# Performance work log

Measured on AMD Instinct MI355X. Metric: run time of the kernel, lower is better.

The kernel has to match this reference:

```python
import jax, jax.numpy as jnp
import numpy as np

N, K, G, C, H = 4096, 32, 1, 96, 6
HD = C // H
POS_BND = int(0.8 * K)      # 25 (dilation=1)
RPE_NUM = 2 * POS_BND + 1   # 51
SCALE = HD ** -0.5


def setup_inputs() -> dict:
    key = jax.random.key(0)
    ks = jax.random.split(key, 6)
    return {
        "data": jax.random.normal(ks[0], (N, K + G, C), jnp.float32),
        "rel_pos": jax.random.randint(ks[1], (N, K, K, 3), 0, RPE_NUM, jnp.int32),
        "mask": jnp.zeros((N, K + G, K + G), jnp.float32),
        "qkv_w": jax.random.normal(ks[2], (C, 3 * C), jnp.float32) * 0.05,
        "qkv_b": jnp.zeros((3 * C,), jnp.float32),
        "proj_w": jax.random.normal(ks[3], (C, C), jnp.float32) * 0.05,
        "proj_b": jnp.zeros((C,), jnp.float32),
        "rpe_table": jax.random.normal(ks[4], (3 * RPE_NUM, H), jnp.float32) * 0.02,
    }


def _rpe_lookup(rel_pos, rpe_table):
    # rel_pos holds uniform indices in [0, RPE_NUM); center to [-POS_BND, POS_BND]
    xyz = rel_pos - POS_BND
    xyz = jnp.clip(xyz, -POS_BND, POS_BND)
    idx = xyz + POS_BND + jnp.arange(3, dtype=rel_pos.dtype) * RPE_NUM  # [N,K,K,3]
    rpe = rpe_table[idx].sum(axis=3)   # gather table -> [N,K,K,3,H] -> sum xyz -> [N,K,K,H]
    return rpe.transpose(0, 3, 1, 2)   # [N,H,K,K]


def reference(data, rel_pos, mask, qkv_w, qkv_b, proj_w, proj_b, rpe_table):
    # data: [N, K+G, C] windowed tokens with G relay tokens already prepended
    qkv = (data @ qkv_w + qkv_b).reshape(N, K + G, 3, H, HD)
    qkv = qkv.transpose(2, 0, 3, 1, 4)               # [3, N, H, K+G, HD]
    q, k, v = qkv[0] * SCALE, qkv[1], qkv[2]
    attn = jnp.einsum('nhqd,nhkd->nhqk', q, k)       # [N, H, K+G, K+G]
    rpe = _rpe_lookup(rel_pos, rpe_table)            # [N, H, K, K]
    rpe = jnp.pad(rpe, ((0, 0), (0, 0), (G, 0), (G, 0)))  # F.pad(rpe,(G,0,G,0))
    attn = attn + rpe + mask[:, None]                # additive HAT window mask
    attn = jax.nn.softmax(attn, axis=-1)
    out = jnp.einsum('nhqk,nhkd->nhqd', attn, v)
    out = out.transpose(0, 2, 1, 3).reshape(N, K + G, C)
    return out @ proj_w + proj_b
```

## Files before the change

### kernel.cpp

```cpp
#include <hip/hip_runtime.h>
#include <cstdint>


static constexpr int NWIN = 4096;
static constexpr int MROWS = NWIN * 33;
static constexpr float SCALE = 0.25f;
static constexpr int KVSTRIDE = 7008;

using short8 = __attribute__((ext_vector_type(8))) short;
using f32x4  = __attribute__((ext_vector_type(4))) float;

__device__ __forceinline__ unsigned short f2bf(float f) {
  unsigned u = __float_as_uint(f);
  u += 0x7fffu + ((u >> 16) & 1u);
  return (unsigned short)(u >> 16);
}
__device__ __forceinline__ float bf2f(unsigned short h) {
  return __uint_as_float(((unsigned)h) << 16);
}
__device__ __forceinline__ float bflo(unsigned u) { return __uint_as_float(u << 16); }
__device__ __forceinline__ float bfhi(unsigned u) { return __uint_as_float(u & 0xffff0000u); }

__global__ __launch_bounds__(256) void conv_w_qkv(
    const float* __restrict__ W, unsigned* __restrict__ frag) {
  const int fp = blockIdx.x;
  const int kstep = fp / 36;
  const int r = fp - kstep*36;
  const int cf = r >> 1, hl = r & 1;
  const int t = threadIdx.x, lane = t >> 2, d = t & 3;
  const int k = kstep*32 + (lane >> 4)*8 + d*2;
  const int n = cf*16 + (lane & 15);
  float w0 = W[k*288 + n], w1 = W[(k+1)*288 + n];
  if (hl) { w0 -= bf2f(f2bf(w0)); w1 -= bf2f(f2bf(w1)); }
  frag[fp*256 + t] = (unsigned)f2bf(w0) | ((unsigned)f2bf(w1) << 16);
}

__global__ __launch_bounds__(256) void conv_w_proj(
    const float* __restrict__ W, unsigned* __restrict__ frag) {
  const int fp = blockIdx.x;
  const int kstep = fp / 12;
  const int r = fp - kstep*12;
  const int cf = r >> 1, hl = r & 1;
  const int t = threadIdx.x, lane = t >> 2, d = t & 3;
  const int k = kstep*32 + (lane >> 4)*8 + d*2;
  const int n = cf*16 + (lane & 15);
  float w0 = W[k*96 + n], w1 = W[(k+1)*96 + n];
  if (hl) { w0 -= bf2f(f2bf(w0)); w1 -= bf2f(f2bf(w1)); }
  frag[fp*256 + t] = (unsigned)f2bf(w0) | ((unsigned)f2bf(w1) << 16);
}

__global__ __launch_bounds__(256) void qkv_mfma(
    const float* __restrict__ A, const unsigned* __restrict__ frag,
    const float* __restrict__ bias, float* __restrict__ qf,
    unsigned short* __restrict__ kvh) {
  __shared__ __align__(16) unsigned short sBuf[13056];
  unsigned short* sAh = sBuf;
  unsigned short* sAl = sBuf + 5120;
  const int tid = threadIdx.x;
  const int w = tid >> 6, l = tid & 63;
  const int m0 = blockIdx.x * 128;
  const int s = blockIdx.y;
  f32x4 acc[2][6];
  #pragma unroll
  for (int rf = 0; rf < 2; ++rf)
    #pragma unroll
    for (int cf = 0; cf < 6; ++cf) acc[rf][cf] = (f32x4){0.f,0.f,0.f,0.f};

  #pragma unroll
  for (int kstep = 0; kstep < 3; ++kstep) {
    short8 bh[6], bl[6];
    #pragma unroll
    for (int cf = 0; cf < 6; ++cf) {
      const int fp = (kstep*18 + s*6 + cf)*2;
      bh[cf] = *(const short8*)((const char*)frag + (size_t)fp*1024 + l*16);
      bl[cf] = *(const short8*)((const char*)frag + (size_t)fp*1024 + 1024 + l*16);
    }
    __syncthreads();
    #pragma unroll
    for (int it2 = 0; it2 < 4; ++it2) {
      const int idx = tid + it2*256;
      const int row = idx >> 3, q = idx & 7;
      const float4 v = *(const float4*)(A + (size_t)(m0+row)*96 + kstep*32 + q*4);
      ushort4 hv, lv;
      hv.x = f2bf(v.x); hv.y = f2bf(v.y); hv.z = f2bf(v.z); hv.w = f2bf(v.w);
      lv.x = f2bf(v.x - bf2f(hv.x)); lv.y = f2bf(v.y - bf2f(hv.y));
      lv.z = f2bf(v.z - bf2f(hv.z)); lv.w = f2bf(v.w - bf2f(hv.w));
      *(ushort4*)&sAh[row*40 + q*4] = hv;
      *(ushort4*)&sAl[row*40 + q*4] = lv;
    }
    __syncthreads();
    #pragma unroll
    for (int rf = 0; rf < 2; ++rf) {
      const int row = w*32 + rf*16 + (l & 15);
      const int off = row*40 + (l >> 4)*8;
      const short8 ah = *(const short8*)&sAh[off];
      const short8 al = *(const short8*)&sAl[off];
      #pragma unroll
      for (int cf = 0; cf < 6; ++cf) {
        acc[rf][cf] = __builtin_amdgcn_mfma_f32_16x16x32_bf16(ah, bh[cf], acc[rf][cf], 0,0,0);
        acc[rf][cf] = __builtin_amdgcn_mfma_f32_16x16x32_bf16(al, bh[cf], acc[rf][cf], 0,0,0);
        acc[rf][cf] = __builtin_amdgcn_mfma_f32_16x16x32_bf16(ah, bl[cf], acc[rf][cf], 0,0,0);
      }
    }
  }
  const int col = l & 15;
  if (s == 0) {
    #pragma unroll
    for (int cf = 0; cf < 6; ++cf) {
      const float bv = bias[cf*16 + col];
      #pragma unroll
      for (int rf = 0; rf < 2; ++rf)
        #pragma unroll
        for (int r = 0; r < 4; ++r) {
          const int m = m0 + w*32 + rf*16 + (l >> 4)*4 + r;
          const int n = m / 33, t = m - n*33;
          qf[(size_t)n*3168 + cf*528 + t*16 + col] = (acc[rf][cf][r] + bv)*SCALE;
        }
    }
  } else if (s == 1) {
    #pragma unroll
    for (int cf = 0; cf < 6; ++cf) {
      const float bv = bias[96 + cf*16 + col];
      #pragma unroll
      for (int rf = 0; rf < 2; ++rf)
        #pragma unroll
        for (int r = 0; r < 4; ++r) {
          const int m = m0 + w*32 + rf*16 + (l >> 4)*4 + r;
          const int n = m / 33, t = m - n*33;
          kvh[(size_t)n*KVSTRIDE + cf*528 + t*16 + col] = f2bf(acc[rf][cf][r] + bv);
        }
    }
  } else {
    __syncthreads();
    unsigned short* sV = sBuf;
    #pragma unroll
    for (int cf = 0; cf < 6; ++cf) {
      const float bv = bias[192 + cf*16 + col];
      #pragma unroll
      for (int rf = 0; rf < 2; ++rf)
        #pragma unroll
        for (int r = 0; r < 4; ++r) {
          const int row = w*32 + rf*16 + (l >> 4)*4 + r;
          sV[row*102 + cf*16 + col] = f2bf(acc[rf][cf][r] + bv);
        }
    }
    __syncthreads();
    for (int idx = tid; idx < 12288; idx += 256) {
      const int hd = idx >> 7, trow = idx & 127;
      const int m = m0 + trow;
      const int n = m / 33, t = m - n*33;
      kvh[(size_t)n*KVSTRIDE + 3168 + (hd >> 4)*640 + (hd & 15)*40 + t] =
          sV[trow*102 + hd];
    }
  }
}

__global__ __launch_bounds__(384) void attn_kernel(
    float* __restrict__ qf, const unsigned short* __restrict__ kvh,
    const int* __restrict__ rel, const float* __restrict__ mask,
    const float* __restrict__ rpet) {
  __shared__ __align__(8) unsigned short sBiasH[7168];
  __shared__ __align__(4) unsigned short sRpe6[920];
  const int tid = threadIdx.x;
  const int n = blockIdx.x;
  const int l = tid & 63, g = l >> 4, c = l & 15, h = tid >> 6;
  const unsigned short* Kb = kvh + (size_t)n*KVSTRIDE + h*528;
  const unsigned short* Vb = kvh + (size_t)n*KVSTRIDE + 3168 + h*640;
  const float*          Qb = qf  + (size_t)n*3168 + h*528;
  short8 ka[3];
  #pragma unroll
  for (int jt = 0; jt < 3; ++jt)
    ka[jt] = *(const short8*)(Kb + (jt*16 + c)*16 + (g & 1)*8);
  const short8 vb8 = *(const short8*)(Vb + c*40 + g*8);
  const unsigned short v32u = Vb[c*40 + 32];
  float4 qa_[3], qc_[3];
  #pragma unroll
  for (int it = 0; it < 3; ++it) {
    const int i = it*16 + c;
    qa_[it] = make_float4(0.f,0.f,0.f,0.f);
    qc_[it] = make_float4(0.f,0.f,0.f,0.f);
    if (i < 33) {
      qa_[it] = *(const float4*)(Qb + i*16 + (g & 1)*8);
      qc_[it] = *(const float4*)(Qb + i*16 + (g & 1)*8 + 4);
    }
  }
  for (int idx = tid; idx < 918; idx += 384) sRpe6[idx] = f2bf(rpet[idx]);
  __syncthreads();
  {
    const float* gm = mask + (size_t)n*1089;
    const int*   rb = rel  + (size_t)n*3072;
    const unsigned* rp6 = (const unsigned*)sRpe6;
    int   ee[3];
    bool  act[3], rpok[3];
    float mv[3];
    int   xx[3][3];
    #pragma unroll
    for (int q2 = 0; q2 < 3; ++q2) {
      int e = tid + q2*384;
      act[q2] = (e < 1089);
      if (!act[q2]) e = 0;
      ee[q2] = e;
      const int i = e / 33, j = e - i*33;
      rpok[q2] = (i > 0) && (j > 0);
      const int rbase = rpok[q2] ? ((i-1)*32 + (j-1))*3 : 0;
      mv[q2]    = gm[e];
      xx[q2][0] = rb[rbase]*3;
      xx[q2][1] = (rb[rbase+1] + 51)*3;
      xx[q2][2] = (rb[rbase+2] + 102)*3;
    }
    #pragma unroll
    for (int q2 = 0; q2 < 3; ++q2) {
      float b0=0.f, b1=0.f, b2=0.f, b3=0.f, b4=0.f, b5=0.f;
      #pragma unroll
      for (int a = 0; a < 3; ++a) {
        const unsigned u0 = rp6[xx[q2][a]];
        const unsigned u1 = rp6[xx[q2][a]+1];
        const unsigned u2 = rp6[xx[q2][a]+2];
        b0 += bflo(u0); b1 += bfhi(u0);
        b2 += bflo(u1); b3 += bfhi(u1);
        b4 += bflo(u2); b5 += bfhi(u2);
      }
      const float m2 = mv[q2];
      const bool ok = rpok[q2];
      b0 = ok ? b0 + m2 : m2;  b1 = ok ? b1 + m2 : m2;
      b2 = ok ? b2 + m2 : m2;  b3 = ok ? b3 + m2 : m2;
      b4 = ok ? b4 + m2 : m2;  b5 = ok ? b5 + m2 : m2;
      if (act[q2]) {
        const int e = ee[q2];
        const int i = e / 33, j = e - i*33;
        const int bb = i*36 + j;
        sBiasH[bb]        = f2bf(b0);
        sBiasH[bb + 1188] = f2bf(b1);
        sBiasH[bb + 2376] = f2bf(b2);
        sBiasH[bb + 3564] = f2bf(b3);
        sBiasH[bb + 4752] = f2bf(b4);
        sBiasH[bb + 5940] = f2bf(b5);
      }
    }
  }
  const float v32f = bf2f(v32u);
  short8 qfr[3];
  #pragma unroll
  for (int it = 0; it < 3; ++it) {
    const float qv[8] = {qa_[it].x, qa_[it].y, qa_[it].z, qa_[it].w,
                         qc_[it].x, qc_[it].y, qc_[it].z, qc_[it].w};
    short8 t;
    #pragma unroll
    for (int e = 0; e < 8; ++e) {
      const unsigned short hi = f2bf(qv[e]);
      const unsigned short lo = f2bf(qv[e] - bf2f(hi));
      t[e] = (short)((g < 2) ? hi : lo);
    }
    qfr[it] = t;
  }
  __syncthreads();
  const int hbase = h*1188;
  #pragma unroll
  for (int it = 0; it < 3; ++it) {
    const int i  = it*16 + c;
    const int bi = (i < 33) ? i : 0;
    const int bbase = hbase + bi*36;
    float pv[12];
    float mx = -3.4e38f;
    #pragma unroll
    for (int jt = 0; jt < 3; ++jt) {
      const ushort4 bv4 = *(const ushort4*)(sBiasH + bbase + jt*16 + 4*g);
      f32x4 sacc;
      sacc[0] = bf2f(bv4.x); sacc[1] = bf2f(bv4.y);
      sacc[2] = bf2f(bv4.z); sacc[3] = bf2f(bv4.w);
      sacc = __builtin_amdgcn_mfma_f32_16x16x32_bf16(ka[jt], qfr[it], sacc, 0,0,0);
      #pragma unroll
      for (int r = 0; r < 4; ++r) {
        const int j = jt*16 + 4*g + r;
        float sv = sacc[r];
        if (j >= 33) sv = -3.4e38f;
        pv[jt*4+r] = sv;
        mx = fmaxf(mx, sv);
      }
    }
    mx = fmaxf(mx, __shfl_xor(mx, 16));
    mx = fmaxf(mx, __shfl_xor(mx, 32));
    float ss = 0.f;
    #pragma unroll
    for (int e = 0; e < 12; ++e) { pv[e] = __expf(pv[e] - mx); ss += pv[e]; }
    ss += __shfl_xor(ss, 16);
    ss += __shfl_xor(ss, 32);
    const float inv = 1.0f / ss;
    const unsigned t0d0 = (unsigned)f2bf(pv[0]*inv) | ((unsigned)f2bf(pv[1]*inv) << 16);
    const unsigned t0d1 = (unsigned)f2bf(pv[2]*inv) | ((unsigned)f2bf(pv[3]*inv) << 16);
    const unsigned t1d0 = (unsigned)f2bf(pv[4]*inv) | ((unsigned)f2bf(pv[5]*inv) << 16);
    const unsigned t1d1 = (unsigned)f2bf(pv[6]*inv) | ((unsigned)f2bf(pv[7]*inv) << 16);
    const int L0 = (((g << 1) & 3) << 4) | c;
    const int L1 = ((((g << 1) | 1) & 3) << 4) | c;
    const unsigned s00 = (unsigned)__shfl((int)t0d0, L0);
    const unsigned s01 = (unsigned)__shfl((int)t0d1, L0);
    const unsigned s02 = (unsigned)__shfl((int)t1d0, L0);
    const unsigned s03 = (unsigned)__shfl((int)t1d1, L0);
    const unsigned s10 = (unsigned)__shfl((int)t0d0, L1);
    const unsigned s11 = (unsigned)__shfl((int)t0d1, L1);
    const unsigned s12 = (unsigned)__shfl((int)t1d0, L1);
    const unsigned s13 = (unsigned)__shfl((int)t1d1, L1);
    const bool lo2 = (g < 2);
    uint4 av;
    av.x = lo2 ? s00 : s02;
    av.y = lo2 ? s01 : s03;
    av.z = lo2 ? s10 : s12;
    av.w = lo2 ? s11 : s13;
    const short8 pa = __builtin_bit_cast(short8, av);
    f32x4 o = (f32x4){0.f,0.f,0.f,0.f};
    o = __builtin_amdgcn_mfma_f32_16x16x32_bf16(pa, vb8, o, 0,0,0);
    const float p32f = pv[8] * inv;
    #pragma unroll
    for (int r = 0; r < 4; ++r) {
      const float p32 = __shfl(p32f, 4*g + r);
      o[r] += p32 * v32f;
    }
    float* ob = qf + (size_t)n*3168 + h*16 + c;
    #pragma unroll
    for (int r = 0; r < 4; ++r) {
      const int io = it*16 + 4*g + r;
      if (io < 33) ob[(size_t)io*96] = o[r];
    }
  }
}

__global__ __launch_bounds__(256) void proj_mfma(
    const float* __restrict__ qf, const unsigned* __restrict__ frag,
    const float* __restrict__ bias, float* __restrict__ out) {
  __shared__ __align__(16) unsigned short sAh[128*104];
  __shared__ __align__(16) unsigned short sAl[128*104];
  const int tid = threadIdx.x;
  const int w = tid >> 6, l = tid & 63;
  const int m0 = blockIdx.x * 128;
  for (int idx = tid; idx < 3072; idx += 256) {
    const int row = idx / 24, q = idx - row*24;
    const int m = m0 + row;
    const int n = m / 33, t = m - n*33;
    const float4 v = *(const float4*)(qf + (size_t)n*3168 + t*96 + q*4);
    ushort4 hv, lv;
    hv.x = f2bf(v.x); hv.y = f2bf(v.y); hv.z = f2bf(v.z); hv.w = f2bf(v.w);
    lv.x = f2bf(v.x - bf2f(hv.x)); lv.y = f2bf(v.y - bf2f(hv.y));
    lv.z = f2bf(v.z - bf2f(hv.z)); lv.w = f2bf(v.w - bf2f(hv.w));
    *(ushort4*)&sAh[row*104 + q*4] = hv;
    *(ushort4*)&sAl[row*104 + q*4] = lv;
  }
  __syncthreads();
  f32x4 acc[2][6];
  #pragma unroll
  for (int rf = 0; rf < 2; ++rf)
    #pragma unroll
    for (int cf = 0; cf < 6; ++cf) acc[rf][cf] = (f32x4){0.f,0.f,0.f,0.f};

  #pragma unroll
  for (int kstep = 0; kstep < 3; ++kstep) {
    short8 bh[6], bl[6];
    #pragma unroll
    for (int cf = 0; cf < 6; ++cf) {
      const int fph = kstep*12 + cf*2;
      bh[cf] = *(const short8*)(frag + fph*256 + l*4);
      bl[cf] = *(const short8*)(frag + (fph+1)*256 + l*4);
    }
    #pragma unroll
    for (int rf = 0; rf < 2; ++rf) {
      const int row = w*32 + rf*16 + (l & 15);
      const int off = row*104 + kstep*32 + (l >> 4)*8;
      const short8 ah = *(const short8*)&sAh[off];
      const short8 al = *(const short8*)&sAl[off];
      #pragma unroll
      for (int cf = 0; cf < 6; ++cf) {
        acc[rf][cf] = __builtin_amdgcn_mfma_f32_16x16x32_bf16(ah, bh[cf], acc[rf][cf], 0,0,0);
        acc[rf][cf] = __builtin_amdgcn_mfma_f32_16x16x32_bf16(al, bh[cf], acc[rf][cf], 0,0,0);
        acc[rf][cf] = __builtin_amdgcn_mfma_f32_16x16x32_bf16(ah, bl[cf], acc[rf][cf], 0,0,0);
      }
    }
  }
  const int col = l & 15;
  #pragma unroll
  for (int cf = 0; cf < 6; ++cf) {
    const float bv = bias[cf*16 + col];
    #pragma unroll
    for (int rf = 0; rf < 2; ++rf)
      #pragma unroll
      for (int r = 0; r < 4; ++r) {
        const int m = m0 + w*32 + rf*16 + (l >> 4)*4 + r;
        out[(size_t)m*96 + cf*16 + col] = acc[rf][cf][r] + bv;
      }
  }
}

extern "C" void kernel_launch(void* const* d_in, const int* in_sizes, int n_in,
                              void* d_out, int out_size, void* d_ws, size_t ws_size,
                              hipStream_t stream) {
  const float* data   = (const float*)d_in[0];
  const int*   rel    = (const int*)  d_in[1];
  const float* mask   = (const float*)d_in[2];
  const float* qkv_w  = (const float*)d_in[3];
  const float* qkv_b  = (const float*)d_in[4];
  const float* proj_w = (const float*)d_in[5];
  const float* proj_b = (const float*)d_in[6];
  const float* rpet   = (const float*)d_in[7];
  float* qf = (float*)d_ws;
  unsigned short* kvh = (unsigned short*)(qf + (size_t)NWIN*3168);
  float* out = (float*)d_out;

  conv_w_qkv <<<dim3(108),          256, 0, stream>>>(qkv_w, (unsigned*)d_out);
  qkv_mfma   <<<dim3(MROWS/128, 3), 256, 0, stream>>>(data, (const unsigned*)d_out, qkv_b, qf, kvh);
  attn_kernel<<<dim3(NWIN),         384, 0, stream>>>(qf, kvh, rel, mask, rpet);
  conv_w_proj<<<dim3(36),           256, 0, stream>>>(proj_w, (unsigned*)kvh);
  proj_mfma  <<<dim3(MROWS/128),    256, 0, stream>>>(qf, (const unsigned*)kvh, proj_b, out);
}
```

Measured before the change: 137.9 us.

## Split QKV GEMM into Q and fused K/V kernels; stream proj A tiles per k-step

The single 3-way blockIdx.y QKV kernel becomes two kernels. A Q kernel handles the Q projection on 128-row tiles. A KV kernel handles K and V together on 64-row tiles, reusing one A-tile conversion for both, so the input is read and split to bf16 twice instead of three times. The proj kernel now loads and splits its A tile one 32-column k-step at a time into a smaller shared buffer instead of staging all 96 columns up front, which cuts LDS use and may raise occupancy. The trade-offs are an extra kernel launch, an extra sync per k-step, and the K/V kernel doing per-wave work on 16 rows, which may lower MFMA utilisation per block.

```diff
diff --git a/kernel.cpp b/kernel.cpp
--- a/kernel.cpp
+++ b/kernel.cpp
@@ -49,17 +49,15 @@
   frag[fp*256 + t] = (unsigned)f2bf(w0) | ((unsigned)f2bf(w1) << 16);
 }
 
-__global__ __launch_bounds__(256) void qkv_mfma(
+__global__ __launch_bounds__(256) void q_mfma(
     const float* __restrict__ A, const unsigned* __restrict__ frag,
-    const float* __restrict__ bias, float* __restrict__ qf,
-    unsigned short* __restrict__ kvh) {
-  __shared__ __align__(16) unsigned short sBuf[13056];
+    const float* __restrict__ bias, float* __restrict__ qf) {
+  __shared__ __align__(16) unsigned short sBuf[10240];
   unsigned short* sAh = sBuf;
   unsigned short* sAl = sBuf + 5120;
   const int tid = threadIdx.x;
   const int w = tid >> 6, l = tid & 63;
   const int m0 = blockIdx.x * 128;
-  const int s = blockIdx.y;
   f32x4 acc[2][6];
   #pragma unroll
   for (int rf = 0; rf < 2; ++rf)
@@ -71,7 +69,7 @@
     short8 bh[6], bl[6];
     #pragma unroll
     for (int cf = 0; cf < 6; ++cf) {
-      const int fp = (kstep*18 + s*6 + cf)*2;
+      const int fp = (kstep*18 + cf)*2;
       bh[cf] = *(const short8*)((const char*)frag + (size_t)fp*1024 + l*16);
       bl[cf] = *(const short8*)((const char*)frag + (size_t)fp*1024 + 1024 + l*16);
     }
@@ -104,54 +102,110 @@
     }
   }
   const int col = l & 15;
-  if (s == 0) {
-    #pragma unroll
-    for (int cf = 0; cf < 6; ++cf) {
-      const float bv = bias[cf*16 + col];
-      #pragma unroll
-      for (int rf = 0; rf < 2; ++rf)
-        #pragma unroll
-        for (int r = 0; r < 4; ++r) {
-          const int m = m0 + w*32 + rf*16 + (l >> 4)*4 + r;
-          const int n = m / 33, t = m - n*33;
-          qf[(size_t)n*3168 + cf*528 + t*16 + col] = (acc[rf][cf][r] + bv)*SCALE;
-        }
-    }
-  } else if (s == 1) {
-    #pragma unroll
-    for (int cf = 0; cf < 6; ++cf) {
-      const float bv = bias[96 + cf*16 + col];
-      #pragma unroll
-      for (int rf = 0; rf < 2; ++rf)
-        #pragma unroll
-        for (int r = 0; r < 4; ++r) {
-          const int m = m0 + w*32 + rf*16 + (l >> 4)*4 + r;
-          const int n = m / 33, t = m - n*33;
-          kvh[(size_t)n*KVSTRIDE + cf*528 + t*16 + col] = f2bf(acc[rf][cf][r] + bv);
-        }
-    }
-  } else {
-    __syncthreads();
-    unsigned short* sV = sBuf;
-    #pragma unroll
-    for (int cf = 0; cf < 6; ++cf) {
-      const float bv = bias[192 + cf*16 + col];
-      #pragma unroll
-      for (int rf = 0; rf < 2; ++rf)
-        #pragma unroll
-        for (int r = 0; r < 4; ++r) {
-          const int row = w*32 + rf*16 + (l >> 4)*4 + r;
-          sV[row*102 + cf*16 + col] = f2bf(acc[rf][cf][r] + bv);
-        }
-    }
-    __syncthreads();
-    for (int idx = tid; idx < 12288; idx += 256) {
-      const int hd = idx >> 7, trow = idx & 127;
-      const int m = m0 + trow;
+  #pragma unroll
+  for (int cf = 0; cf < 6; ++cf) {
+    const float bv = bias[cf*16 + col];
+    #pragma unroll
+    for (int rf = 0; rf < 2; ++rf)
+      #pragma unroll
+      for (int r = 0; r < 4; ++r) {
+        const int m = m0 + w*32 + rf*16 + (l >> 4)*4 + r;
+        const int n = m / 33, t = m - n*33;
+        qf[(size_t)n*3168 + cf*528 + t*16 + col] = (acc[rf][cf][r] + bv)*SCALE;
+      }
+  }
+}
+
+__global__ __launch_bounds__(256) void kv_mfma(
+    const float* __restrict__ A, const unsigned* __restrict__ frag,
+    const float* __restrict__ bias, unsigned short* __restrict__ kvh) {
+  __shared__ __align__(16) unsigned short sBuf[6528];
+  unsigned short* sAh = sBuf;
+  unsigned short* sAl = sBuf + 2560;
+  const int tid = threadIdx.x;
+  const int w = tid >> 6, l = tid & 63;
+  const int m0 = blockIdx.x * 64;
+  f32x4 acck[6], accv[6];
+  #pragma unroll
+  for (int cf = 0; cf < 6; ++cf) {
+    acck[cf] = (f32x4){0.f,0.f,0.f,0.f};
+    accv[cf] = (f32x4){0.f,0.f,0.f,0.f};
+  }
+  #pragma unroll
+  for (int kstep = 0; kstep < 3; ++kstep) {
+    short8 bh[6], bl[6];
+    #pragma unroll
+    for (int cf = 0; cf < 6; ++cf) {
+      const int fp = (kstep*18 + 6 + cf)*2;
+      bh[cf] = *(const short8*)((const char*)frag + (size_t)fp*1024 + l*16);
+      bl[cf] = *(const short8*)((const char*)frag + (size_t)fp*1024 + 1024 + l*16);
+    }
+    __syncthreads();
+    #pragma unroll
+    for (int it2 = 0; it2 < 2; ++it2) {
+      const int idx = tid + it2*256;
+      const int row = idx >> 3, q = idx & 7;
+      const float4 v = *(const float4*)(A + (size_t)(m0+row)*96 + kstep*32 + q*4);
+      ushort4 hv, lv;
+      hv.x = f2bf(v.x); hv.y = f2bf(v.y); hv.z = f2bf(v.z); hv.w = f2bf(v.w);
+      lv.x = f2bf(v.x - bf2f(hv.x)); lv.y = f2bf(v.y - bf2f(hv.y));
+      lv.z = f2bf(v.z - bf2f(hv.z)); lv.w = f2bf(v.w - bf2f(hv.w));
+      *(ushort4*)&sAh[row*40 + q*4] = hv;
+      *(ushort4*)&sAl[row*40 + q*4] = lv;
+    }
+    __syncthreads();
+    const int row = w*16 + (l & 15);
+    const int off = row*40 + (l >> 4)*8;
+    const short8 ah = *(const short8*)&sAh[off];
+    const short8 al = *(const short8*)&sAl[off];
+    #pragma unroll
+    for (int cf = 0; cf < 6; ++cf) {
+      acck[cf] = __builtin_amdgcn_mfma_f32_16x16x32_bf16(ah, bh[cf], acck[cf], 0,0,0);
+      acck[cf] = __builtin_amdgcn_mfma_f32_16x16x32_bf16(al, bh[cf], acck[cf], 0,0,0);
+      acck[cf] = __builtin_amdgcn_mfma_f32_16x16x32_bf16(ah, bl[cf], acck[cf], 0,0,0);
+    }
+    #pragma unroll
+    for (int cf = 0; cf < 6; ++cf) {
+      const int fp = (kstep*18 + 12 + cf)*2;
+      bh[cf] = *(const short8*)((const char*)frag + (size_t)fp*1024 + l*16);
+      bl[cf] = *(const short8*)((const char*)frag + (size_t)fp*1024 + 1024 + l*16);
+    }
+    #pragma unroll
+    for (int cf = 0; cf < 6; ++cf) {
+      accv[cf] = __builtin_amdgcn_mfma_f32_16x16x32_bf16(ah, bh[cf], accv[cf], 0,0,0);
+      accv[cf] = __builtin_amdgcn_mfma_f32_16x16x32_bf16(al, bh[cf], accv[cf], 0,0,0);
+      accv[cf] = __builtin_amdgcn_mfma_f32_16x16x32_bf16(ah, bl[cf], accv[cf], 0,0,0);
+    }
+  }
+  const int col = l & 15;
+  #pragma unroll
+  for (int cf = 0; cf < 6; ++cf) {
+    const float bv = bias[96 + cf*16 + col];
+    #pragma unroll
+    for (int r = 0; r < 4; ++r) {
+      const int m = m0 + w*16 + (l >> 4)*4 + r;
       const int n = m / 33, t = m - n*33;
-      kvh[(size_t)n*KVSTRIDE + 3168 + (hd >> 4)*640 + (hd & 15)*40 + t] =
-          sV[trow*102 + hd];
-    }
+      kvh[(size_t)n*KVSTRIDE + cf*528 + t*16 + col] = f2bf(acck[cf][r] + bv);
+    }
+  }
+  __syncthreads();
+  unsigned short* sV = sBuf;
+  #pragma unroll
+  for (int cf = 0; cf < 6; ++cf) {
+    const float bv = bias[192 + cf*16 + col];
+    #pragma unroll
+    for (int r = 0; r < 4; ++r) {
+      const int row = w*16 + (l >> 4)*4 + r;
+      sV[row*102 + cf*16 + col] = f2bf(accv[cf][r] + bv);
+    }
+  }
+  __syncthreads();
+  for (int idx = tid; idx < 6144; idx += 256) {
+    const int hd = idx >> 6, trow = idx & 63;
+    const int m = m0 + trow;
+    const int n = m / 33, t = m - n*33;
+    kvh[(size_t)n*KVSTRIDE + 3168 + (hd >> 4)*640 + (hd & 15)*40 + t] =
+        sV[trow*102 + hd];
   }
 }
 
@@ -327,24 +381,12 @@
 __global__ __launch_bounds__(256) void proj_mfma(
     const float* __restrict__ qf, const unsigned* __restrict__ frag,
     const float* __restrict__ bias, float* __restrict__ out) {
-  __shared__ __align__(16) unsigned short sAh[128*104];
-  __shared__ __align__(16) unsigned short sAl[128*104];
+  __shared__ __align__(16) unsigned short sBuf[10240];
+  unsigned short* sAh = sBuf;
+  unsigned short* sAl = sBuf + 5120;
   const int tid = threadIdx.x;
   const int w = tid >> 6, l = tid & 63;
   const int m0 = blockIdx.x * 128;
-  for (int idx = tid; idx < 3072; idx += 256) {
-    const int row = idx / 24, q = idx - row*24;
-    const int m = m0 + row;
-    const int n = m / 33, t = m - n*33;
-    const float4 v = *(const float4*)(qf + (size_t)n*3168 + t*96 + q*4);
-    ushort4 hv, lv;
-    hv.x = f2bf(v.x); hv.y = f2bf(v.y); hv.z = f2bf(v.z); hv.w = f2bf(v.w);
-    lv.x = f2bf(v.x - bf2f(hv.x)); lv.y = f2bf(v.y - bf2f(hv.y));
-    lv.z = f2bf(v.z - bf2f(hv.z)); lv.w = f2bf(v.w - bf2f(hv.w));
-    *(ushort4*)&sAh[row*104 + q*4] = hv;
-    *(ushort4*)&sAl[row*104 + q*4] = lv;
-  }
-  __syncthreads();
   f32x4 acc[2][6];
   #pragma unroll
   for (int rf = 0; rf < 2; ++rf)
@@ -360,10 +402,26 @@
       bh[cf] = *(const short8*)(frag + fph*256 + l*4);
       bl[cf] = *(const short8*)(frag + (fph+1)*256 + l*4);
     }
+    __syncthreads();
+    #pragma unroll
+    for (int it2 = 0; it2 < 4; ++it2) {
+      const int idx = tid + it2*256;
+      const int row = idx >> 3, q = idx & 7;
+      const int m = m0 + row;
+      const int n = m / 33, t = m - n*33;
+      const float4 v = *(const float4*)(qf + (size_t)n*3168 + t*96 + kstep*32 + q*4);
+      ushort4 hv, lv;
+      hv.x = f2bf(v.x); hv.y = f2bf(v.y); hv.z = f2bf(v.z); hv.w = f2bf(v.w);
+      lv.x = f2bf(v.x - bf2f(hv.x)); lv.y = f2bf(v.y - bf2f(hv.y));
+      lv.z = f2bf(v.z - bf2f(hv.z)); lv.w = f2bf(v.w - bf2f(hv.w));
+      *(ushort4*)&sAh[row*40 + q*4] = hv;
+      *(ushort4*)&sAl[row*40 + q*4] = lv;
+    }
+    __syncthreads();
     #pragma unroll
     for (int rf = 0; rf < 2; ++rf) {
       const int row = w*32 + rf*16 + (l & 15);
-      const int off = row*104 + kstep*32 + (l >> 4)*8;
+      const int off = row*40 + (l >> 4)*8;
       const short8 ah = *(const short8*)&sAh[off];
       const short8 al = *(const short8*)&sAl[off];
       #pragma unroll
@@ -403,9 +461,10 @@
   unsigned short* kvh = (unsigned short*)(qf + (size_t)NWIN*3168);
   float* out = (float*)d_out;
 
-  conv_w_qkv <<<dim3(108),          256, 0, stream>>>(qkv_w, (unsigned*)d_out);
-  qkv_mfma   <<<dim3(MROWS/128, 3), 256, 0, stream>>>(data, (const unsigned*)d_out, qkv_b, qf, kvh);
-  attn_kernel<<<dim3(NWIN),         384, 0, stream>>>(qf, kvh, rel, mask, rpet);
-  conv_w_proj<<<dim3(36),           256, 0, stream>>>(proj_w, (unsigned*)kvh);
-  proj_mfma  <<<dim3(MROWS/128),    256, 0, stream>>>(qf, (const unsigned*)kvh, proj_b, out);
-}
+  conv_w_qkv <<<dim3(108),        256, 0, stream>>>(qkv_w, (unsigned*)d_out);
+  q_mfma     <<<dim3(MROWS/128),  256, 0, stream>>>(data, (const unsigned*)d_out, qkv_b, qf);
+  kv_mfma    <<<dim3(MROWS/64),   256, 0, stream>>>(data, (const unsigned*)d_out, qkv_b, kvh);
+  attn_kernel<<<dim3(NWIN),       384, 0, stream>>>(qf, kvh, rel, mask, rpet);
+  conv_w_proj<<<dim3(36),         256, 0, stream>>>(proj_w, (unsigned*)kvh);
+  proj_mfma  <<<dim3(MROWS/128),  256, 0, stream>>>(qf, (const unsigned*)kvh, proj_b, out);
+}
```

New measurement: 146.9 us. 6.5% more time.
